# Kernel tuning notes

Hardware: AMD Instinct MI355X
Metric: run time of the kernel (lower is better)

## Reference

```python
import jax, jax.numpy as jnp
import numpy as np

B, T, D_MODEL = 2, 2048, 2048
NUM_HEADS, NUM_KV_HEADS, HEAD_DIM = 16, 16, 128
NUM_Q_HEADS = 2 * NUM_HEADS  # diff-v2 doubles the query heads


def _rope_freqs(seqlen, dim_half, base=10000.0):
    inv = 1.0 / (base ** (np.arange(0, dim_half, dtype=np.float32) / dim_half))
    t = np.arange(seqlen, dtype=np.float32)
    ang = np.outer(t, inv)  # [T, dim_half]
    return jnp.asarray(np.cos(ang)), jnp.asarray(np.sin(ang))


def apply_rotary_interleaved(x, cos, sin):
    # x: [B, T, H, D]; cos/sin: [T, D//2]; pairs are adjacent (interleaved=True)
    x1, x2 = x[..., 0::2], x[..., 1::2]
    c = cos[None, :, None, :]
    s = sin[None, :, None, :]
    o1 = x1 * c - x2 * s
    o2 = x1 * s + x2 * c
    return jnp.stack([o1, o2], axis=-1).reshape(x.shape)


def setup_inputs() -> dict:
    key = jax.random.key(0)
    ks = jax.random.split(key, 6)
    x = jax.random.normal(ks[0], (B, T, D_MODEL), dtype=jnp.float32)
    cos, sin = _rope_freqs(T, HEAD_DIM // 2)
    sc = 1.0 / np.sqrt(D_MODEL)
    Wq = jax.random.normal(ks[1], (D_MODEL, NUM_Q_HEADS * HEAD_DIM), dtype=jnp.float32) * sc
    Wk = jax.random.normal(ks[2], (D_MODEL, NUM_KV_HEADS * HEAD_DIM), dtype=jnp.float32) * sc
    Wv = jax.random.normal(ks[3], (D_MODEL, NUM_KV_HEADS * HEAD_DIM), dtype=jnp.float32) * sc
    Wo = jax.random.normal(ks[4], (NUM_HEADS * HEAD_DIM, D_MODEL), dtype=jnp.float32) * sc
    Wlam = jax.random.normal(ks[5], (D_MODEL, NUM_HEADS), dtype=jnp.float32) * sc
    return {"x": x, "cos": cos, "sin": sin, "Wq": Wq, "Wk": Wk, "Wv": Wv, "Wo": Wo, "Wlam": Wlam}


def reference(x, cos, sin, Wq, Wk, Wv, Wo, Wlam):
    b, t, _ = x.shape
    q = (x @ Wq).reshape(b, t, NUM_Q_HEADS, HEAD_DIM)
    k = (x @ Wk).reshape(b, t, NUM_KV_HEADS, HEAD_DIM)
    v = (x @ Wv).reshape(b, t, NUM_KV_HEADS, HEAD_DIM)
    q = apply_rotary_interleaved(q, cos, sin)
    k = apply_rotary_interleaved(k, cos, sin)
    # GQA: repeat kv heads to match the doubled query heads
    rep = NUM_Q_HEADS // NUM_KV_HEADS
    k = jnp.repeat(k, rep, axis=2)
    v = jnp.repeat(v, rep, axis=2)
    scale = 1.0 / np.sqrt(HEAD_DIM)
    scores = jnp.einsum('bthd,bshd->bhts', q, k) * scale  # [B, 2H, T, T]
    causal = jnp.tril(jnp.ones((t, t), dtype=bool))
    scores = jnp.where(causal[None, None], scores, jnp.finfo(scores.dtype).min)
    p = jax.nn.softmax(scores, axis=-1)
    attn = jnp.einsum('bhts,bshd->bthd', p, v)  # [B, T, 2H, D]
    lam = jax.nn.sigmoid(x @ Wlam)  # [B, T, H]
    attn1, attn2 = attn[:, :, 0::2], attn[:, :, 1::2]
    out = attn1 - lam[..., None] * attn2  # [B, T, H, D]
    return out.reshape(b, t, NUM_HEADS * HEAD_DIM) @ Wo
```

## Files before the change

### kernel.cpp

```cpp
#include <hip/hip_runtime.h>

#define T_SEQ 2048
#define BATCH 2
#define DMODEL 2048
#define NQH 32
#define NKVH 16
#define HD 128

typedef _Float16 f16;
typedef _Float16 f16x8 __attribute__((ext_vector_type(8)));
typedef _Float16 f16x4 __attribute__((ext_vector_type(4)));
typedef _Float16 f16x2 __attribute__((ext_vector_type(2)));
typedef float f32x4 __attribute__((ext_vector_type(4)));

typedef const __attribute__((address_space(1))) void* gptr_t;
typedef __attribute__((address_space(3))) void* sptr_t;
#define GLDS16(g, l) __builtin_amdgcn_global_load_lds((gptr_t)(g), (sptr_t)(l), 16, 0, 0)

__global__ __launch_bounds__(256) void k_transpose_all(const float* __restrict__ Wq,
                                                       const float* __restrict__ Wk,
                                                       const float* __restrict__ Wv,
                                                       const float* __restrict__ Wo,
                                                       f16* __restrict__ WqkvT,
                                                       f16* __restrict__ WoT) {
  __shared__ float tile[32][33];
  const int z = blockIdx.z;
  const float* W;
  f16* WT;
  int N;
  if (z == 0)      { W = Wq; WT = WqkvT;                          N = 4096; }
  else if (z == 1) { W = Wk; WT = WqkvT + (size_t)4096 * 2048;    N = 2048; }
  else if (z == 2) { W = Wv; WT = WqkvT + (size_t)6144 * 2048;    N = 2048; }
  else             { W = Wo; WT = WoT;                            N = 2048; }
  const int K = 2048;
  int n0 = blockIdx.x * 32;
  if (n0 >= N) return;
  int k0 = blockIdx.y * 32;
  int tx = threadIdx.x & 31;
  int ty0 = threadIdx.x >> 5;
  #pragma unroll
  for (int i = 0; i < 4; ++i) {
    int ty = ty0 + i * 8;
    tile[ty][tx] = W[(size_t)(k0 + ty) * N + n0 + tx];
  }
  __syncthreads();
  #pragma unroll
  for (int i = 0; i < 4; ++i) {
    int ty = ty0 + i * 8;
    WT[(size_t)(n0 + ty) * K + k0 + tx] = (f16)tile[tx][ty];
  }
}

__global__ __launch_bounds__(512, 1) void k_gemm8p(const f16* __restrict__ A,
                                                   const f16* __restrict__ BT,
                                                   f16* __restrict__ Qh,
                                                   f16* __restrict__ Kh,
                                                   f16* __restrict__ VTg,
                                                   const float* __restrict__ cosb,
                                                   const float* __restrict__ sinb) {
  const int K = 2048, N = 8192;
  __shared__ alignas(16) f16 Al[2][256 * 64];
  __shared__ alignas(16) f16 Bl[2][256 * 64];
  const int tid = threadIdx.x;
  const int lane = tid & 63;
  const int w = tid >> 6;
  const int wr = w >> 2, wc = w & 3;
  const int lr = lane & 15, lg = lane >> 4;
  const int nbx = 32;
  const int cpx = gridDim.x >> 3;
  const int wg = (blockIdx.x & 7) * cpx + (blockIdx.x >> 3);
  const int m0 = (wg / nbx) * 256, n0 = (wg % nbx) * 256;

#define ST_A(MH, BB, KK)                                                        \
  { _Pragma("unroll")                                                           \
    for (int i2 = 0; i2 < 2; ++i2) {                                            \
      int li = i2 * 512 + tid; int rh = li >> 3, g = li & 7;                    \
      int r = ((rh >> 6) << 7) + (MH) * 64 + (rh & 63);                         \
      GLDS16(A + (size_t)(m0 + r) * K + (KK) + ((g ^ (r & 7)) * 8),             \
             &Al[BB][(r * 8 + g) * 8]);                                         \
    } }
#define ST_B(NH, BB, KK)                                                        \
  { _Pragma("unroll")                                                           \
    for (int i2 = 0; i2 < 2; ++i2) {                                            \
      int li = i2 * 512 + tid; int rh = li >> 3, g = li & 7;                    \
      int r = ((rh >> 5) << 6) + (NH) * 32 + (rh & 31);                         \
      GLDS16(BT + (size_t)(n0 + r) * K + (KK) + ((g ^ (r & 7)) * 8),            \
             &Bl[BB][(r * 8 + g) * 8]);                                         \
    } }
#define LDA_Q(MH, BUF)                                                          \
  { _Pragma("unroll")                                                           \
    for (int kh = 0; kh < 2; ++kh)                                              \
      _Pragma("unroll")                                                         \
      for (int i = 0; i < 4; ++i) {                                             \
        int r = wr * 128 + ((MH) * 4 + i) * 16 + lr;                            \
        af[kh][i] = *(const f16x8*)&Al[BUF][r * 64 + (((kh * 4 + lg) ^ (r & 7)) * 8)]; \
      } }
#define LDB_Q(NH, BUF)                                                          \
  { _Pragma("unroll")                                                           \
    for (int kh = 0; kh < 2; ++kh)                                              \
      _Pragma("unroll")                                                         \
      for (int j = 0; j < 2; ++j) {                                             \
        int r = wc * 64 + ((NH) * 2 + j) * 16 + lr;                             \
        bf[kh][j] = *(const f16x8*)&Bl[BUF][r * 64 + (((kh * 4 + lg) ^ (r & 7)) * 8)]; \
      } }
#define FMA_Q(MH, NH)                                                           \
  { __builtin_amdgcn_s_setprio(1);                                              \
    _Pragma("unroll")                                                           \
    for (int kh = 0; kh < 2; ++kh)                                              \
      _Pragma("unroll")                                                         \
      for (int i = 0; i < 4; ++i)                                               \
        _Pragma("unroll")                                                       \
        for (int j = 0; j < 2; ++j)                                             \
          acc[(MH) * 4 + i][(NH) * 2 + j] = __builtin_amdgcn_mfma_f32_16x16x32_f16( \
              af[kh][i], bf[kh][j], acc[(MH) * 4 + i][(NH) * 2 + j], 0, 0, 0);  \
    __builtin_amdgcn_s_setprio(0); }
#define BAR() __builtin_amdgcn_s_barrier()
#define SB() __builtin_amdgcn_sched_barrier(0)
#define LGKM0() { asm volatile("s_waitcnt lgkmcnt(0)" ::: "memory"); SB(); }

  f32x4 acc[8][4] = {};
  ST_A(0, 0, 0); ST_B(0, 0, 0); ST_B(1, 0, 0); ST_A(1, 0, 0);
  asm volatile("s_waitcnt vmcnt(4)" ::: "memory");
  BAR();

  const int nt = K / 64;
  #pragma unroll 2
  for (int t = 0; t < nt; ++t) {
    const int buf = t & 1;
    const int kk1 = (t + 1) * 64;
    const bool nxt = (t + 1 < nt);
    f16x8 af[2][4], bf[2][2];
    LDA_Q(0, buf); LDB_Q(0, buf);
    if (nxt) ST_A(0, buf ^ 1, kk1);
    BAR(); LGKM0();
    FMA_Q(0, 0);
    if (nxt) { asm volatile("s_waitcnt vmcnt(4)" ::: "memory"); }
    else     { asm volatile("s_waitcnt vmcnt(2)" ::: "memory"); }
    SB(); BAR(); SB();
    LDB_Q(1, buf);
    if (nxt) ST_B(0, buf ^ 1, kk1);
    BAR(); LGKM0();
    FMA_Q(0, 1);
    if (nxt) { asm volatile("s_waitcnt vmcnt(4)" ::: "memory"); }
    else     { asm volatile("s_waitcnt vmcnt(0)" ::: "memory"); }
    SB(); BAR(); SB();
    LDA_Q(1, buf); LDB_Q(0, buf);
    if (nxt) ST_B(1, buf ^ 1, kk1);
    BAR(); LGKM0();
    FMA_Q(1, 0);
    SB(); BAR(); SB();
    LDB_Q(1, buf);
    if (nxt) ST_A(1, buf ^ 1, kk1);
    BAR(); LGKM0();
    FMA_Q(1, 1);
    if (nxt) { asm volatile("s_waitcnt vmcnt(4)" ::: "memory"); }
    SB(); BAR(); SB();
  }
#undef ST_A
#undef ST_B
#undef LDA_Q
#undef LDB_Q
#undef FMA_Q
#undef BAR
#undef SB
#undef LGKM0

  const int mb = m0 + wr * 128;
  const int nb = n0 + wc * 64;
  if (n0 < 6144) {
    f16* dst = (n0 < 4096) ? Qh : Kh;
    const int ncols = (n0 < 4096) ? 4096 : 2048;
    const int coff = (n0 < 4096) ? 0 : 4096;
    #pragma unroll
    for (int i = 0; i < 8; ++i)
      #pragma unroll
      for (int j = 0; j < 4; ++j) {
        int c = nb + j * 16 + lr - coff;
        int jp = (c & 127) >> 1;
        bool odd = (c & 1);
        #pragma unroll
        for (int r = 0; r < 4; ++r) {
          int row = mb + i * 16 + lg * 4 + r;
          int t = row & (T_SEQ - 1);
          float v = acc[i][j][r];
          float pv = __shfl_xor(v, 1);
          float cs = cosb[t * 64 + jp], sn = sinb[t * 64 + jp];
          float out = odd ? (pv * sn + v * cs) : (v * cs - pv * sn);
          dst[(size_t)row * ncols + c] = (f16)out;
        }
      }
  } else {
    #pragma unroll
    for (int i = 0; i < 8; ++i)
      #pragma unroll
      for (int j = 0; j < 4; ++j) {
        int c = nb + j * 16 + lr - 6144;
        int head = c >> 7, d = c & 127;
        int row0 = mb + i * 16 + lg * 4;
        int bb = row0 >> 11, t0 = row0 & (T_SEQ - 1);
        f16x4 zv;
        #pragma unroll
        for (int r = 0; r < 4; ++r) zv[r] = (f16)acc[i][j][r];
        *(f16x4*)(VTg + ((size_t)(bb * NKVH + head) * HD + d) * T_SEQ + t0) = zv;
      }
  }
}

template<int BM, int BN, int WM, int WN, int THREADS>
__global__ __launch_bounds__(THREADS, 2) void k_gemm2(const f16* __restrict__ A,
                                                      const f16* __restrict__ BT,
                                                      float* __restrict__ C,
                                                      int M, int N, int K) {
  constexpr int MR = BM / WM / 16;
  constexpr int NR = BN / WN / 16;
  constexpr int ACH = BM * 64 / 8 / THREADS;
  constexpr int BCH = BN * 64 / 8 / THREADS;
  static_assert(ACH + BCH == 8, "vmcnt constant assumes 8 loads/thread/stage");
  __shared__ alignas(16) f16 Al[2][BM * 64];
  __shared__ alignas(16) f16 Bl[2][BN * 64];
  const int tid = threadIdx.x;
  const int lane = tid & 63;
  const int w = tid >> 6;
  const int wr = w / WN, wc = w % WN;
  const int lr = lane & 15, lg = lane >> 4;
  const int nbx = N / BN;
  const int cpx = gridDim.x >> 3;
  const int wg = (blockIdx.x & 7) * cpx + (blockIdx.x >> 3);
  const int m0 = (wg / nbx) * BM, n0 = (wg % nbx) * BN;

  auto STAGE = [&](int buf, int kk) {
    #pragma unroll
    for (int q = 0; q < ACH; ++q) {
      int idx = q * THREADS + tid;
      int r = idx >> 3, g = idx & 7;
      GLDS16(A + (size_t)(m0 + r) * K + kk + ((g ^ (r & 7)) * 8), &Al[buf][idx * 8]);
    }
    #pragma unroll
    for (int q = 0; q < BCH; ++q) {
      int idx = q * THREADS + tid;
      int r = idx >> 3, g = idx & 7;
      GLDS16(BT + (size_t)(n0 + r) * K + kk + ((g ^ (r & 7)) * 8), &Bl[buf][idx * 8]);
    }
  };

  f32x4 acc[MR][NR] = {};
  STAGE(0, 0);
  const int nt = K / 64;
  #pragma unroll 2
  for (int t = 0; t < nt; ++t) {
    const int buf = t & 1;
    if (t + 1 < nt) {
      STAGE(buf ^ 1, (t + 1) * 64);
      __builtin_amdgcn_sched_barrier(0);
      asm volatile("s_waitcnt vmcnt(8)" ::: "memory");
    } else {
      __builtin_amdgcn_sched_barrier(0);
      asm volatile("s_waitcnt vmcnt(0)" ::: "memory");
    }
    __builtin_amdgcn_s_barrier();
    __builtin_amdgcn_sched_barrier(0);
    #pragma unroll
    for (int kh = 0; kh < 2; ++kh) {
      f16x8 af[MR], bf[NR];
      #pragma unroll
      for (int i = 0; i < MR; ++i) {
        int r = wr * (BM / WM) + i * 16 + lr;
        af[i] = *(const f16x8*)&Al[buf][r * 64 + (((kh * 4 + lg) ^ (r & 7)) * 8)];
      }
      #pragma unroll
      for (int j = 0; j < NR; ++j) {
        int r = wc * (BN / WN) + j * 16 + lr;
        bf[j] = *(const f16x8*)&Bl[buf][r * 64 + (((kh * 4 + lg) ^ (r & 7)) * 8)];
      }
      #pragma unroll
      for (int i = 0; i < MR; ++i)
        #pragma unroll
        for (int j = 0; j < NR; ++j)
          acc[i][j] = __builtin_amdgcn_mfma_f32_16x16x32_f16(af[i], bf[j], acc[i][j], 0, 0, 0);
    }
    __builtin_amdgcn_sched_barrier(0);
    __builtin_amdgcn_s_barrier();
    __builtin_amdgcn_sched_barrier(0);
  }

  const int mb = m0 + wr * (BM / WM);
  const int nb = n0 + wc * (BN / WN);
  #pragma unroll
  for (int i = 0; i < MR; ++i)
    #pragma unroll
    for (int j = 0; j < NR; ++j) {
      int r0 = mb + i * 16 + lg * 4;
      int c = nb + j * 16 + lr;
      #pragma unroll
      for (int r = 0; r < 4; ++r)
        C[(size_t)(r0 + r) * N + c] = acc[i][j][r];
    }
}

__global__ __launch_bounds__(256) void k_lambda_conv(const float* __restrict__ x,
                                                     const float* __restrict__ Wlam,
                                                     float* __restrict__ lam,
                                                     f16* __restrict__ xh) {
  int row = blockIdx.x;
  const float* xr = x + (size_t)row * DMODEL;
  const int e = threadIdx.x * 8;
  const float4* xp = (const float4*)(xr + e);
  float4 a = xp[0], b2 = xp[1];
  float xv[8] = {a.x, a.y, a.z, a.w, b2.x, b2.y, b2.z, b2.w};
  f16x8 hv;
  #pragma unroll
  for (int j = 0; j < 8; ++j) hv[j] = (f16)xv[j];
  *(f16x8*)(xh + (size_t)row * DMODEL + e) = hv;
  float acc[16];
  #pragma unroll
  for (int h = 0; h < 16; ++h) acc[h] = 0.f;
  #pragma unroll
  for (int j = 0; j < 8; ++j) {
    const float4* wp = (const float4*)(Wlam + (size_t)(e + j) * 16);
    #pragma unroll
    for (int g = 0; g < 4; ++g) {
      float4 wv = wp[g];
      acc[g * 4 + 0] += xv[j] * wv.x; acc[g * 4 + 1] += xv[j] * wv.y;
      acc[g * 4 + 2] += xv[j] * wv.z; acc[g * 4 + 3] += xv[j] * wv.w;
    }
  }
  #pragma unroll
  for (int h = 0; h < 16; ++h)
    for (int off = 32; off > 0; off >>= 1)
      acc[h] += __shfl_down(acc[h], off);
  __shared__ float part[4][16];
  int lane = threadIdx.x & 63, w = threadIdx.x >> 6;
  if (lane == 0) {
    #pragma unroll
    for (int h = 0; h < 16; ++h) part[w][h] = acc[h];
  }
  __syncthreads();
  if (threadIdx.x < 16) {
    float s = part[0][threadIdx.x] + part[1][threadIdx.x] + part[2][threadIdx.x] + part[3][threadIdx.x];
    lam[row * 16 + threadIdx.x] = 1.f / (1.f + __expf(-s));
  }
}

__global__ __launch_bounds__(512, 4) void k_attn6(const f16* __restrict__ Q,
                                                  const f16* __restrict__ K,
                                                  const f16* __restrict__ VT,
                                                  const float* __restrict__ lam,
                                                  f16* __restrict__ Z) {
  __shared__ f16 Kl[64 * 128];
  __shared__ f16 Vl[128 * 64];
  __shared__ f16 Pl[8][16][40];
  __shared__ f16 Po[4][16][136];
  const int tid = threadIdx.x;
  const int lane = tid & 63;
  const int w = tid >> 6;
  const int lr = lane & 15, lg = lane >> 4;
  const int flat = blockIdx.x;
  const int xcd = flat & 7;
  const int work = xcd * 64 + (flat >> 3);
  const int grp = work >> 4;
  const int bx = work & 15;
  const int b = grp >> 4, hkv = grp & 15;
  const int h = hkv * 2 + (w >> 2);
  const int wq = w & 3;
  const int kvstride = NKVH * HD;
  const f16* Kg  = K  + (size_t)b * T_SEQ * kvstride + hkv * HD;
  const f16* VTg = VT + (size_t)(b * NKVH + hkv) * HD * T_SEQ;
  const float sc = 0.08838834764831845f;

  #pragma unroll 1
  for (int half = 0; half < 2; ++half) {
    const int qt = half ? (31 - bx) : bx;
    const int qb = qt * 64;
    const int qw = qb + wq * 16;
    const int qrow = qw + lr;
    f16x8 qf[4];
    {
      const f16* qp = Q + (size_t)(b * T_SEQ + qrow) * (NQH * HD) + h * HD + lg * 8;
      #pragma unroll
      for (int c = 0; c < 4; ++c) qf[c] = *(const f16x8*)(qp + c * 32);
    }
    f32x4 o[8] = {};
    float mi = -1e30f, li = 0.f;

    const int nt = qt + 1;
    #pragma unroll
    for (int q = 0; q < 2; ++q) {
      int idx = q * 512 + tid;
      int r = idx >> 4, g = idx & 15;
      GLDS16(Kg + (size_t)r * kvstride + (g ^ (r & 7)) * 8, &Kl[idx * 8]);
    }
    #pragma unroll
    for (int q = 0; q < 2; ++q) {
      int idx = q * 512 + tid;
      int d = idx >> 3, g = idx & 7;
      GLDS16(VTg + (size_t)d * T_SEQ + (g ^ (d & 7)) * 8, &Vl[idx * 8]);
    }
    __syncthreads();

    #pragma unroll 1
    for (int t = 0; t < nt; ++t) {
      const int s0 = t * 64;
      const bool pf = (t + 1 < nt);
      f16x8 ka[2], va[2];
      if (pf) {
        const int s1 = s0 + 64;
        #pragma unroll
        for (int q = 0; q < 2; ++q) {
          int idx = q * 512 + tid;
          int r = idx >> 4, g = idx & 15;
          ka[q] = *(const f16x8*)(Kg + (size_t)(s1 + r) * kvstride + g * 8);
        }
        #pragma unroll
        for (int q = 0; q < 2; ++q) {
          int idx = q * 512 + tid;
          int d = idx >> 3, g = idx & 7;
          va[q] = *(const f16x8*)(VTg + (size_t)d * T_SEQ + s1 + g * 8);
        }
      }
      f32x4 sf[4] = {};
      __builtin_amdgcn_s_setprio(1);
      #pragma unroll
      for (int c = 0; c < 4; ++c) {
        #pragma unroll
        for (int nb = 0; nb < 4; ++nb) {
          f16x8 kf = *(const f16x8*)&Kl[(((nb * 16 + lr) * 16) + ((c * 4 + lg) ^ (lr & 7))) * 8];
          sf[nb] = __builtin_amdgcn_mfma_f32_16x16x32_f16(kf, qf[c], sf[nb], 0, 0, 0);
        }
      }
      __builtin_amdgcn_s_setprio(0);
      float v[16];
      #pragma unroll
      for (int nb = 0; nb < 4; ++nb)
        #pragma unroll
        for (int rr = 0; rr < 4; ++rr) {
          float x = sf[nb][rr] * sc;
          int kv = s0 + nb * 16 + lg * 4 + rr;
          v[nb * 4 + rr] = (kv > qrow) ? -1e30f : x;
        }
      float pm = v[0];
      #pragma unroll
      for (int i = 1; i < 16; ++i) pm = fmaxf(pm, v[i]);
      pm = fmaxf(pm, __shfl_xor(pm, 16));
      pm = fmaxf(pm, __shfl_xor(pm, 32));
      const bool nogrow = (__all(pm <= mi + 8.0f) != 0);
      const float mnew = nogrow ? mi : fmaxf(mi, pm);
      float rs = 0.f;
      #pragma unroll
      for (int i = 0; i < 16; ++i) { float p = __expf(v[i] - mnew); v[i] = p; rs += p; }
      rs += __shfl_xor(rs, 16);
      rs += __shfl_xor(rs, 32);
      if (nogrow) {
        li += rs;
      } else {
        float a = __expf(mi - mnew);
        mi = mnew;
        li = a * li + rs;
        float ab[4];
        #pragma unroll
        for (int rr = 0; rr < 4; ++rr) ab[rr] = __shfl(a, lg * 4 + rr);
        #pragma unroll
        for (int j = 0; j < 8; ++j)
          #pragma unroll
          for (int rr = 0; rr < 4; ++rr) o[j][rr] *= ab[rr];
      }
      #pragma unroll
      for (int ks = 0; ks < 2; ++ks) {
        #pragma unroll
        for (int nb2 = 0; nb2 < 2; ++nb2) {
          int nb = ks * 2 + nb2;
          f16x4 pk;
          #pragma unroll
          for (int rr = 0; rr < 4; ++rr) pk[rr] = (f16)v[nb * 4 + rr];
          *(f16x4*)&Pl[w][lr][nb2 * 16 + lg * 4] = pk;
        }
        f16x8 pa = *(const f16x8*)&Pl[w][lr][lg * 8];
        __builtin_amdgcn_s_setprio(1);
        #pragma unroll
        for (int j = 0; j < 8; ++j) {
          f16x8 vbj = *(const f16x8*)&Vl[(((j * 16 + lr) * 8) + ((ks * 4 + lg) ^ (lr & 7))) * 8];
          o[j] = __builtin_amdgcn_mfma_f32_16x16x32_f16(pa, vbj, o[j], 0, 0, 0);
        }
        __builtin_amdgcn_s_setprio(0);
      }
      __syncthreads();
      if (pf) {
        #pragma unroll
        for (int q = 0; q < 2; ++q) {
          int idx = q * 512 + tid;
          int r = idx >> 4, g = idx & 15;
          *(f16x8*)&Kl[(r * 16 + (g ^ (r & 7))) * 8] = ka[q];
        }
        #pragma unroll
        for (int q = 0; q < 2; ++q) {
          int idx = q * 512 + tid;
          int d = idx >> 3, g = idx & 7;
          *(f16x8*)&Vl[(d * 8 + (g ^ (d & 7))) * 8] = va[q];
        }
      }
      __syncthreads();
    }
    float lib[4];
    #pragma unroll
    for (int rr = 0; rr < 4; ++rr) lib[rr] = 1.f / __shfl(li, lg * 4 + rr);
    if (w >= 4) {
      #pragma unroll
      for (int j = 0; j < 8; ++j)
        #pragma unroll
        for (int rr = 0; rr < 4; ++rr)
          Po[wq][lg * 4 + rr][j * 16 + lr] = (f16)(o[j][rr] * lib[rr]);
    }
    __syncthreads();
    if (w < 4) {
      float lamv[4];
      #pragma unroll
      for (int rr = 0; rr < 4; ++rr)
        lamv[rr] = lam[(size_t)(b * T_SEQ + qw + lg * 4 + rr) * 16 + hkv];
      #pragma unroll
      for (int j = 0; j < 8; ++j)
        #pragma unroll
        for (int rr = 0; rr < 4; ++rr) {
          float a1 = o[j][rr] * lib[rr];
          float a2 = (float)Po[wq][lg * 4 + rr][j * 16 + lr];
          Z[(size_t)(b * T_SEQ + qw + lg * 4 + rr) * 2048 + hkv * 128 + j * 16 + lr] =
              (f16)(a1 - lamv[rr] * a2);
        }
    }
    __syncthreads();
  }
}

extern "C" void kernel_launch(void* const* d_in, const int* in_sizes, int n_in,
                              void* d_out, int out_size, void* d_ws, size_t ws_size,
                              hipStream_t stream) {
  const float* x    = (const float*)d_in[0];
  const float* cosb = (const float*)d_in[1];
  const float* sinb = (const float*)d_in[2];
  const float* Wq   = (const float*)d_in[3];
  const float* Wk   = (const float*)d_in[4];
  const float* Wv   = (const float*)d_in[5];
  const float* Wo   = (const float*)d_in[6];
  const float* Wlam = (const float*)d_in[7];

  char* ws = (char*)d_ws;
  f16*  xh     = (f16*)(ws);
  f16*  WqkvT  = (f16*)(ws + 16777216);
  f16*  WoT    = (f16*)(ws + 50331648);
  f16*  Qh     = (f16*)(ws + 58720256);
  f16*  Kh     = (f16*)(ws + 92274688);
  f16*  VTg    = (f16*)(ws + 109051904);
  f16*  Zh     = (f16*)(ws + 159383552);
  float* lam   = (float*)(ws + 176160768);

  k_transpose_all<<<dim3(128, 64, 4), 256, 0, stream>>>(Wq, Wk, Wv, Wo, WqkvT, WoT);
  k_lambda_conv<<<4096, 256, 0, stream>>>(x, Wlam, lam, xh);

  k_gemm8p<<<512, 512, 0, stream>>>(xh, WqkvT, Qh, Kh, VTg, cosb, sinb);

  k_attn6<<<512, 512, 0, stream>>>(Qh, Kh, VTg, lam, Zh);

  k_gemm2<128, 128, 2, 2, 256><<<512, 256, 0, stream>>>(Zh, WoT, (float*)d_out,
                                                        4096, 2048, 2048);
}
```

Measured before the change: 422.8 us.

## Fold softmax scale into Q, use exp2, compute row sums via MFMA

The softmax scale times log2(e) is folded into the Q fragments once, so scores feed exp2f directly with no per-element multiply. Causal masking is skipped for tiles entirely below the diagonal. The row-sum reduction (shuffles plus serial adds) is replaced by an extra MFMA of P against a vector of ones, accumulated like O. The risks are lost precision from scaling Q in fp16, one extra MFMA per k-step, and a rescale threshold re-expressed in the base-2 domain.

```diff
diff --git a/kernel.cpp b/kernel.cpp
--- a/kernel.cpp
+++ b/kernel.cpp
@@ -341,7 +341,7 @@
   }
 }
 
-__global__ __launch_bounds__(512, 4) void k_attn6(const f16* __restrict__ Q,
+__global__ __launch_bounds__(512, 4) void k_attn7(const f16* __restrict__ Q,
                                                   const f16* __restrict__ K,
                                                   const f16* __restrict__ VT,
                                                   const float* __restrict__ lam,
@@ -365,7 +365,10 @@
   const int kvstride = NKVH * HD;
   const f16* Kg  = K  + (size_t)b * T_SEQ * kvstride + hkv * HD;
   const f16* VTg = VT + (size_t)(b * NKVH + hkv) * HD * T_SEQ;
-  const float sc = 0.08838834764831845f;
+  const f16 qsc = (f16)0.12753102f;
+  f16x8 vones;
+  #pragma unroll
+  for (int e2 = 0; e2 < 8; ++e2) vones[e2] = (f16)1.0f;
 
   #pragma unroll 1
   for (int half = 0; half < 2; ++half) {
@@ -377,10 +380,15 @@
     {
       const f16* qp = Q + (size_t)(b * T_SEQ + qrow) * (NQH * HD) + h * HD + lg * 8;
       #pragma unroll
-      for (int c = 0; c < 4; ++c) qf[c] = *(const f16x8*)(qp + c * 32);
+      for (int c = 0; c < 4; ++c) {
+        qf[c] = *(const f16x8*)(qp + c * 32);
+        #pragma unroll
+        for (int e2 = 0; e2 < 8; ++e2) qf[c][e2] = qf[c][e2] * qsc;
+      }
     }
     f32x4 o[8] = {};
-    float mi = -1e30f, li = 0.f;
+    f32x4 osum = {};
+    float mi = -1e30f;
 
     const int nt = qt + 1;
     #pragma unroll
@@ -432,29 +440,29 @@
       #pragma unroll
       for (int nb = 0; nb < 4; ++nb)
         #pragma unroll
-        for (int rr = 0; rr < 4; ++rr) {
-          float x = sf[nb][rr] * sc;
-          int kv = s0 + nb * 16 + lg * 4 + rr;
-          v[nb * 4 + rr] = (kv > qrow) ? -1e30f : x;
-        }
-      float pm = v[0];
-      #pragma unroll
-      for (int i = 1; i < 16; ++i) pm = fmaxf(pm, v[i]);
+        for (int rr = 0; rr < 4; ++rr) v[nb * 4 + rr] = sf[nb][rr];
+      if (s0 + 63 > qw) {
+        #pragma unroll
+        for (int nb = 0; nb < 4; ++nb)
+          #pragma unroll
+          for (int rr = 0; rr < 4; ++rr) {
+            int kv = s0 + nb * 16 + lg * 4 + rr;
+            if (kv > qrow) v[nb * 4 + rr] = -1e30f;
+          }
+      }
+      float m1 = fmaxf(fmaxf(v[0], v[1]), v[2]);
+      float m2 = fmaxf(fmaxf(v[3], v[4]), v[5]);
+      float m3 = fmaxf(fmaxf(v[6], v[7]), v[8]);
+      float m4 = fmaxf(fmaxf(v[9], v[10]), v[11]);
+      float m5 = fmaxf(fmaxf(v[12], v[13]), v[14]);
+      float pm = fmaxf(fmaxf(fmaxf(m1, m2), m3), fmaxf(fmaxf(m4, m5), v[15]));
       pm = fmaxf(pm, __shfl_xor(pm, 16));
       pm = fmaxf(pm, __shfl_xor(pm, 32));
-      const bool nogrow = (__all(pm <= mi + 8.0f) != 0);
+      const bool nogrow = (__all(pm <= mi + 11.5416f) != 0);
       const float mnew = nogrow ? mi : fmaxf(mi, pm);
-      float rs = 0.f;
-      #pragma unroll
-      for (int i = 0; i < 16; ++i) { float p = __expf(v[i] - mnew); v[i] = p; rs += p; }
-      rs += __shfl_xor(rs, 16);
-      rs += __shfl_xor(rs, 32);
-      if (nogrow) {
-        li += rs;
-      } else {
-        float a = __expf(mi - mnew);
+      if (!nogrow) {
+        float a = exp2f(mi - mnew);
         mi = mnew;
-        li = a * li + rs;
         float ab[4];
         #pragma unroll
         for (int rr = 0; rr < 4; ++rr) ab[rr] = __shfl(a, lg * 4 + rr);
@@ -462,7 +470,11 @@
         for (int j = 0; j < 8; ++j)
           #pragma unroll
           for (int rr = 0; rr < 4; ++rr) o[j][rr] *= ab[rr];
-      }
+        #pragma unroll
+        for (int rr = 0; rr < 4; ++rr) osum[rr] *= ab[rr];
+      }
+      #pragma unroll
+      for (int i = 0; i < 16; ++i) v[i] = exp2f(v[i] - mnew);
       #pragma unroll
       for (int ks = 0; ks < 2; ++ks) {
         #pragma unroll
@@ -480,6 +492,7 @@
           f16x8 vbj = *(const f16x8*)&Vl[(((j * 16 + lr) * 8) + ((ks * 4 + lg) ^ (lr & 7))) * 8];
           o[j] = __builtin_amdgcn_mfma_f32_16x16x32_f16(pa, vbj, o[j], 0, 0, 0);
         }
+        osum = __builtin_amdgcn_mfma_f32_16x16x32_f16(pa, vones, osum, 0, 0, 0);
         __builtin_amdgcn_s_setprio(0);
       }
       __syncthreads();
@@ -501,7 +514,7 @@
     }
     float lib[4];
     #pragma unroll
-    for (int rr = 0; rr < 4; ++rr) lib[rr] = 1.f / __shfl(li, lg * 4 + rr);
+    for (int rr = 0; rr < 4; ++rr) lib[rr] = 1.f / osum[rr];
     if (w >= 4) {
       #pragma unroll
       for (int j = 0; j < 8; ++j)
@@ -556,7 +569,7 @@
 
   k_gemm8p<<<512, 512, 0, stream>>>(xh, WqkvT, Qh, Kh, VTg, cosb, sinb);
 
-  k_attn6<<<512, 512, 0, stream>>>(Qh, Kh, VTg, lam, Zh);
+  k_attn7<<<512, 512, 0, stream>>>(Qh, Kh, VTg, lam, Zh);
 
   k_gemm2<128, 128, 2, 2, 256><<<512, 256, 0, stream>>>(Zh, WoT, (float*)d_out,
                                                         4096, 2048, 2048);
```

Result: no change. 422.6 us (-0.0%).
